# Kernel optimization log

Measured on AMD Instinct MI355X. Metric: run time of the kernel, lower is better.

Reference implementation:

```python
import jax, jax.numpy as jnp
import numpy as np

N_NODES = 50000

def setup_inputs() -> dict:
    key = jax.random.key(0)
    k1, k2, k3, k4, k5 = jax.random.split(key, 5)
    x = jax.random.normal(k1, (50000, 128), dtype=jnp.float32)
    weight = jax.random.normal(k2, (128, 32), dtype=jnp.float32) * (np.sqrt(6.0 / (128 + 32)))
    edge_src = jax.random.randint(k3, (1600000,), 0, N_NODES, dtype=jnp.int32)
    edge_dst = jax.random.randint(k4, (1600000,), 0, N_NODES, dtype=jnp.int32)
    edge_weight = jax.random.uniform(k5, (1600000,), dtype=jnp.float32)
    return {"x": x, "weight": weight, "edge_src": edge_src,
            "edge_dst": edge_dst, "edge_weight": edge_weight}

def reference(x, weight, edge_src, edge_dst, edge_weight):
    # h = x @ W  (dense GEMM)
    h = x @ weight                                   # [N, out]
    # out = spmm(adj, h): gather h rows at src, scale by edge weight,
    # scatter-add into dst rows (COO SpMM).
    msgs = edge_weight[:, None] * h[edge_src]        # [E, out]
    out = jax.ops.segment_sum(msgs, edge_dst, num_segments=N_NODES)
    return out
```

## Files before the change

### kernel.cpp

```cpp
#include <hip/hip_runtime.h>
#include <hip/hip_bf16.h>
#include <stdint.h>

#define N_NODES   50000
#define K_DIM     128
#define OUT_DIM   32
#define N_EDGES   1600000
#define NBKT      782
#define CAP       3072
#define AFIT      16
#define FB        ((N_EDGES + 256*AFIT - 1) / (256*AFIT))
#define GB        ((N_NODES + 63) / 64)
#define XSTR      136

typedef __attribute__((ext_vector_type(8))) short bf16x8;
typedef __attribute__((ext_vector_type(4))) float f32x4;

__global__ __launch_bounds__(256) void zero_cursor(int* __restrict__ cursor) {
    for (int i = threadIdx.x; i < NBKT; i += 256) cursor[i] = 0;
}

__global__ __launch_bounds__(256) void gemm_fill(const float* __restrict__ x,
                                                 const float* __restrict__ w,
                                                 __hip_bfloat16* __restrict__ h,
                                                 const int*   __restrict__ esrc,
                                                 const int*   __restrict__ edst,
                                                 const float* __restrict__ ew,
                                                 int*         __restrict__ cursor,
                                                 uint64_t*    __restrict__ pairs) {
    __shared__ __align__(16) char smem[40192];
    const int t = threadIdx.x;

    if (blockIdx.x < FB) {
        int*      cnt   = (int*)smem;
        int*      wbase = (int*)(smem + 3200);
        int*      scr   = (int*)(smem + 6400);
        uint64_t* stg   = (uint64_t*)(smem + 7424);

        for (int i = t; i < 800; i += 256) cnt[i] = 0;
        __syncthreads();

        uint32_t lo[AFIT], hi[AFIT];
        uint16_t rk[AFIT];
        const int base = blockIdx.x * 256 * AFIT;
        #pragma unroll
        for (int k = 0; k < AFIT; ++k) {
            const int e = base + k * 256 + t;
            if (e < N_EDGES) {
                const uint32_t s = (uint32_t)esrc[e];
                const uint32_t d = (uint32_t)edst[e];
                lo[k] = (d << 16) | s;
                hi[k] = __float_as_uint(ew[e]);
                rk[k] = (uint16_t)atomicAdd(&cnt[d >> 6], 1);
            } else {
                lo[k] = 0xffffffffu;
            }
        }
        __syncthreads();
        for (int i = t; i < NBKT; i += 256) {
            const int c = cnt[i];
            if (c) wbase[i] = atomicAdd(&cursor[i], c);
        }
        __syncthreads();
        int v0[4]; int lsum = 0;
        #pragma unroll
        for (int j = 0; j < 4; ++j) { v0[j] = (t * 4 + j < 800) ? cnt[t * 4 + j] : 0; lsum += v0[j]; }
        scr[t] = lsum;
        __syncthreads();
        #pragma unroll
        for (int d = 1; d < 256; d <<= 1) {
            const int a = (t >= d) ? scr[t - d] : 0;
            __syncthreads();
            scr[t] += a;
            __syncthreads();
        }
        int run = scr[t] - lsum;
        #pragma unroll
        for (int j = 0; j < 4; ++j) {
            if (t * 4 + j < 800) { const int c = v0[j]; cnt[t * 4 + j] = run; run += c; }
        }
        __syncthreads();
        #pragma unroll
        for (int k = 0; k < AFIT; ++k) {
            if (lo[k] != 0xffffffffu) {
                const int b = (int)(lo[k] >> 22);
                stg[cnt[b] + (int)rk[k]] = ((uint64_t)hi[k] << 32) | lo[k];
            }
        }
        __syncthreads();
        const int total = min(256 * AFIT, N_EDGES - base);
        for (int i = t; i < total; i += 256) {
            const uint64_t p = stg[i];
            const int b    = (int)((p >> 22) & 0x3ff);
            const int gpos = wbase[b] + i - cnt[b];
            if (gpos < CAP)
                pairs[(size_t)b * CAP + gpos] = p;
        }
    } else {
        uint16_t* wt = (uint16_t*)smem;
        uint16_t* xt = (uint16_t*)(smem + 8704);

        for (int i = t; i < K_DIM * OUT_DIM; i += 256) {
            const int k = i >> 5, c = i & 31;
            const __hip_bfloat16 bv = __float2bfloat16(w[i]);
            wt[c * XSTR + k] = *(const uint16_t*)&bv;
        }
        const int row0 = (blockIdx.x - FB) * 64;
        const float4* xg4 = reinterpret_cast<const float4*>(x);
        const long long gmax4 = (long long)N_NODES * (K_DIM / 4);
        #pragma unroll
        for (int i = 0; i < 8; ++i) {
            const int idx = i * 256 + t;
            const int row = idx >> 5;
            const int k4  = idx & 31;
            const long long gi = (long long)(row0 + row) * (K_DIM / 4) + k4;
            float4 v = make_float4(0.f, 0.f, 0.f, 0.f);
            if (gi < gmax4) v = xg4[gi];
            __hip_bfloat16 b0 = __float2bfloat16(v.x), b1 = __float2bfloat16(v.y);
            __hip_bfloat16 b2 = __float2bfloat16(v.z), b3 = __float2bfloat16(v.w);
            ushort4 u;
            u.x = *(const uint16_t*)&b0; u.y = *(const uint16_t*)&b1;
            u.z = *(const uint16_t*)&b2; u.w = *(const uint16_t*)&b3;
            *reinterpret_cast<ushort4*>(xt + row * XSTR + k4 * 4) = u;
        }
        __syncthreads();

        const int wv   = t >> 6;
        const int lane = t & 63;
        const int m    = lane & 15;
        const int kg   = lane >> 4;

        f32x4 acc0 = {0.f, 0.f, 0.f, 0.f};
        f32x4 acc1 = {0.f, 0.f, 0.f, 0.f};
        const uint16_t* arow = xt + (wv * 16 + m) * XSTR;
        const uint16_t* b0p  = wt + m * XSTR;
        const uint16_t* b1p  = wt + (16 + m) * XSTR;
        #pragma unroll
        for (int s = 0; s < 4; ++s) {
            const int k0 = s * 32 + kg * 8;
            const bf16x8 a  = *reinterpret_cast<const bf16x8*>(arow + k0);
            const bf16x8 b0 = *reinterpret_cast<const bf16x8*>(b0p + k0);
            const bf16x8 b1 = *reinterpret_cast<const bf16x8*>(b1p + k0);
            acc0 = __builtin_amdgcn_mfma_f32_16x16x32_bf16(a, b0, acc0, 0, 0, 0);
            acc1 = __builtin_amdgcn_mfma_f32_16x16x32_bf16(a, b1, acc1, 0, 0, 0);
        }
        #pragma unroll
        for (int r = 0; r < 4; ++r) {
            const int grow = row0 + wv * 16 + kg * 4 + r;
            if (grow < N_NODES) {
                h[(size_t)grow * OUT_DIM + m]      = __float2bfloat16(acc0[r]);
                h[(size_t)grow * OUT_DIM + 16 + m] = __float2bfloat16(acc1[r]);
            }
        }
    }
}

__global__ __launch_bounds__(512) void sort_pull(const int*      __restrict__ cursor,
                                                 const uint64_t* __restrict__ pairs,
                                                 const __hip_bfloat16* __restrict__ h,
                                                 float*          __restrict__ out) {
    __shared__ uint64_t stg[CAP];
    __shared__ int lcnt[64];
    __shared__ int loff[65];
    const int b    = blockIdx.x;
    const int t    = threadIdx.x;
    const size_t beg = (size_t)b * CAP;
    const int cnt  = min(cursor[b], CAP);
    const int wv   = t >> 6;
    const int lane = t & 63;
    const int cp   = lane & 15;
    const int q    = lane >> 4;

    if (t < 64) lcnt[t] = 0;
    __syncthreads();

    uint64_t pl[6];
    int      pr[6];
    #pragma unroll
    for (int k = 0; k < 6; ++k) {
        const int i = t + k * 512;
        if (i < cnt) {
            const uint64_t p = pairs[beg + i];
            const int nl = (int)((p >> 16) & 63);
            pl[k] = p;
            pr[k] = (nl << 12) | atomicAdd(&lcnt[nl], 1);
        } else {
            pr[k] = -1;
        }
    }
    __syncthreads();
    if (t < 64) {
        const int v = lcnt[t];
        int p = v;
        #pragma unroll
        for (int d = 1; d < 64; d <<= 1) {
            const int n = __shfl_up(p, d, 64);
            if (t >= d) p += n;
        }
        loff[t] = p - v;
        if (t == 63) loff[64] = p;
    }
    __syncthreads();
    #pragma unroll
    for (int k = 0; k < 6; ++k) {
        if (pr[k] >= 0)
            stg[loff[pr[k] >> 12] + (pr[k] & 0xfff)] = pl[k];
    }
    __syncthreads();

    const uint32_t* h32 = reinterpret_cast<const uint32_t*>(h);
    for (int nl = wv * 8; nl < wv * 8 + 8; ++nl) {
        const int node = (b << 6) + nl;
        if (node >= N_NODES) break;
        const int jb = loff[nl], je = loff[nl + 1];
        float ax = 0.f, ay = 0.f;
        int j = jb + q;
        for (; j + 12 < je; j += 16) {
            const uint64_t p0 = stg[j];
            const uint64_t p1 = stg[j + 4];
            const uint64_t p2 = stg[j + 8];
            const uint64_t p3 = stg[j + 12];
            const uint32_t v0 = h32[(size_t)(p0 & 0xffffu) * 16 + cp];
            const uint32_t v1 = h32[(size_t)(p1 & 0xffffu) * 16 + cp];
            const uint32_t v2 = h32[(size_t)(p2 & 0xffffu) * 16 + cp];
            const uint32_t v3 = h32[(size_t)(p3 & 0xffffu) * 16 + cp];
            const float w0 = __uint_as_float((uint32_t)(p0 >> 32));
            const float w1 = __uint_as_float((uint32_t)(p1 >> 32));
            const float w2 = __uint_as_float((uint32_t)(p2 >> 32));
            const float w3 = __uint_as_float((uint32_t)(p3 >> 32));
            ax += w0 * __uint_as_float(v0 << 16);
            ay += w0 * __uint_as_float(v0 & 0xffff0000u);
            ax += w1 * __uint_as_float(v1 << 16);
            ay += w1 * __uint_as_float(v1 & 0xffff0000u);
            ax += w2 * __uint_as_float(v2 << 16);
            ay += w2 * __uint_as_float(v2 & 0xffff0000u);
            ax += w3 * __uint_as_float(v3 << 16);
            ay += w3 * __uint_as_float(v3 & 0xffff0000u);
        }
        for (; j < je; j += 4) {
            const uint64_t p = stg[j];
            const uint32_t v = h32[(size_t)(p & 0xffffu) * 16 + cp];
            const float w = __uint_as_float((uint32_t)(p >> 32));
            ax += w * __uint_as_float(v << 16);
            ay += w * __uint_as_float(v & 0xffff0000u);
        }
        ax += __shfl_xor(ax, 16, 64);  ay += __shfl_xor(ay, 16, 64);
        ax += __shfl_xor(ax, 32, 64);  ay += __shfl_xor(ay, 32, 64);
        if (q == 0) {
            float2* o2 = reinterpret_cast<float2*>(out + (size_t)node * OUT_DIM);
            o2[cp] = make_float2(ax, ay);
        }
    }
}

__global__ __launch_bounds__(256) void gemm_only(const float* __restrict__ x,
                                                 const float* __restrict__ w,
                                                 __hip_bfloat16* __restrict__ h) {
    __shared__ float wlds[K_DIM * OUT_DIM];
    const int t = threadIdx.x;
    #pragma unroll
    for (int i = 0; i < (K_DIM * OUT_DIM) / 256; ++i)
        wlds[i * 256 + t] = w[i * 256 + t];
    __syncthreads();
    const int row = blockIdx.x * 8 + (t >> 5);
    const int col = t & 31;
    if (row >= N_NODES) return;
    const float4* x4 = reinterpret_cast<const float4*>(x + (size_t)row * K_DIM);
    float acc = 0.f;
    #pragma unroll
    for (int k4 = 0; k4 < K_DIM / 4; ++k4) {
        float4 xv = x4[k4];
        const int k = k4 * 4;
        acc += xv.x * wlds[(k + 0) * OUT_DIM + col] + xv.y * wlds[(k + 1) * OUT_DIM + col]
             + xv.z * wlds[(k + 2) * OUT_DIM + col] + xv.w * wlds[(k + 3) * OUT_DIM + col];
    }
    h[(size_t)row * OUT_DIM + col] = __float2bfloat16(acc);
}

__global__ __launch_bounds__(256) void scatter_kernel(const int*   __restrict__ esrc,
                                                      const int*   __restrict__ edst,
                                                      const float* __restrict__ ew,
                                                      const __hip_bfloat16* __restrict__ h,
                                                      float*       out) {
    const long long gid = (long long)blockIdx.x * blockDim.x + threadIdx.x;
    const int e   = (int)(gid >> 5);
    const int col = (int)(gid & 31);
    if (e >= N_EDGES) return;
    atomicAdd(out + (size_t)edst[e] * OUT_DIM + col,
              ew[e] * __bfloat162float(h[(size_t)esrc[e] * OUT_DIM + col]));
}

extern "C" void kernel_launch(void* const* d_in, const int* in_sizes, int n_in,
                              void* d_out, int out_size, void* d_ws, size_t ws_size,
                              hipStream_t stream) {
    const float* x    = (const float*)d_in[0];
    const float* w    = (const float*)d_in[1];
    const int*   esrc = (const int*)d_in[2];
    const int*   edst = (const int*)d_in[3];
    const float* ew   = (const float*)d_in[4];
    float*       out  = (float*)d_out;

    const size_t PAIRS_B = (size_t)NBKT * CAP * 8;
    const size_t H_B     = (size_t)N_NODES * OUT_DIM * 2;
    const size_t CUR_B   = (size_t)NBKT * 4;
    const size_t REQ     = PAIRS_B + H_B + CUR_B;

    uint64_t*        pairs  = (uint64_t*)d_ws;
    __hip_bfloat16*  h      = (__hip_bfloat16*)((char*)d_ws + PAIRS_B);
    int*             cursor = (int*)((char*)d_ws + PAIRS_B + H_B);

    if (ws_size >= REQ) {
        zero_cursor<<<1, 256, 0, stream>>>(cursor);
        gemm_fill<<<FB + GB, 256, 0, stream>>>(x, w, h, esrc, edst, ew, cursor, pairs);
        sort_pull<<<NBKT, 512, 0, stream>>>(cursor, pairs, h, out);
    } else {
        __hip_bfloat16* hf = (__hip_bfloat16*)d_ws;
        (void)hipMemsetAsync(d_out, 0, (size_t)out_size * sizeof(float), stream);
        gemm_only<<<(N_NODES + 7) / 8, 256, 0, stream>>>(x, w, hf);
        const long long total = (long long)N_EDGES * OUT_DIM;
        scatter_kernel<<<(int)((total + 255) / 256), 256, 0, stream>>>(esrc, edst, ew, hf, out);
    }
}
```

Measured before the change: 52.15 us.

## Fuse all stages into one persistent cooperative kernel with grid syncs

Replaces the three launches (zero cursor, gemm+fill, sort+pull) with a single cooperative kernel that loops over work items and uses grid-wide syncs between phases. Blocks grow to 512 threads, fill handles 4096 edges per item, and the GEMM splits output columns across waves. This removes per-launch overhead and inter-kernel gaps. In exchange it adds grid.sync cost, restricts the grid to the number of resident blocks (perCU*256), and drops the low-workspace fallback path.

```diff
diff --git a/kernel.cpp b/kernel.cpp
--- a/kernel.cpp
+++ b/kernel.cpp
@@ -1,6 +1,9 @@
 #include <hip/hip_runtime.h>
+#include <hip/hip_cooperative_groups.h>
 #include <hip/hip_bf16.h>
 #include <stdint.h>
+
+namespace cg = cooperative_groups;
 
 #define N_NODES   50000
 #define K_DIM     128
@@ -8,162 +11,151 @@
 #define N_EDGES   1600000
 #define NBKT      782
 #define CAP       3072
-#define AFIT      16
-#define FB        ((N_EDGES + 256*AFIT - 1) / (256*AFIT))
-#define GB        ((N_NODES + 63) / 64)
+#define FB        391
+#define GI        782
 #define XSTR      136
+#define SMEM_B    41216
 
 typedef __attribute__((ext_vector_type(8))) short bf16x8;
 typedef __attribute__((ext_vector_type(4))) float f32x4;
 
-__global__ __launch_bounds__(256) void zero_cursor(int* __restrict__ cursor) {
-    for (int i = threadIdx.x; i < NBKT; i += 256) cursor[i] = 0;
-}
-
-__global__ __launch_bounds__(256) void gemm_fill(const float* __restrict__ x,
-                                                 const float* __restrict__ w,
-                                                 __hip_bfloat16* __restrict__ h,
-                                                 const int*   __restrict__ esrc,
-                                                 const int*   __restrict__ edst,
-                                                 const float* __restrict__ ew,
-                                                 int*         __restrict__ cursor,
-                                                 uint64_t*    __restrict__ pairs) {
-    __shared__ __align__(16) char smem[40192];
-    const int t = threadIdx.x;
-
-    if (blockIdx.x < FB) {
-        int*      cnt   = (int*)smem;
-        int*      wbase = (int*)(smem + 3200);
-        int*      scr   = (int*)(smem + 6400);
-        uint64_t* stg   = (uint64_t*)(smem + 7424);
-
-        for (int i = t; i < 800; i += 256) cnt[i] = 0;
+__device__ void fill_item(int item, char* smem, int t,
+                          const int* __restrict__ esrc, const int* __restrict__ edst,
+                          const float* __restrict__ ew, int* __restrict__ cursor,
+                          uint64_t* __restrict__ pairs) {
+    int*      cnt   = (int*)smem;
+    int*      wbase = (int*)(smem + 3200);
+    int*      scr   = (int*)(smem + 6400);
+    uint64_t* stg   = (uint64_t*)(smem + 8448);
+
+    __syncthreads();
+    for (int i = t; i < 800; i += 512) cnt[i] = 0;
+    __syncthreads();
+
+    uint32_t lo[8], hi[8];
+    uint16_t rk[8];
+    const int base = item * 4096;
+    #pragma unroll
+    for (int k = 0; k < 8; ++k) {
+        const int e = base + k * 512 + t;
+        if (e < N_EDGES) {
+            const uint32_t s = (uint32_t)esrc[e];
+            const uint32_t d = (uint32_t)edst[e];
+            lo[k] = (d << 16) | s;
+            hi[k] = __float_as_uint(ew[e]);
+            rk[k] = (uint16_t)atomicAdd(&cnt[d >> 6], 1);
+        } else {
+            lo[k] = 0xffffffffu;
+        }
+    }
+    __syncthreads();
+    for (int i = t; i < NBKT; i += 512) {
+        const int c = cnt[i];
+        if (c) wbase[i] = atomicAdd(&cursor[i], c);
+    }
+    __syncthreads();
+    int v0[2]; int lsum = 0;
+    #pragma unroll
+    for (int j = 0; j < 2; ++j) { v0[j] = (t * 2 + j < 800) ? cnt[t * 2 + j] : 0; lsum += v0[j]; }
+    scr[t] = lsum;
+    __syncthreads();
+    #pragma unroll
+    for (int d = 1; d < 512; d <<= 1) {
+        const int a = (t >= d) ? scr[t - d] : 0;
         __syncthreads();
-
-        uint32_t lo[AFIT], hi[AFIT];
-        uint16_t rk[AFIT];
-        const int base = blockIdx.x * 256 * AFIT;
-        #pragma unroll
-        for (int k = 0; k < AFIT; ++k) {
-            const int e = base + k * 256 + t;
-            if (e < N_EDGES) {
-                const uint32_t s = (uint32_t)esrc[e];
-                const uint32_t d = (uint32_t)edst[e];
-                lo[k] = (d << 16) | s;
-                hi[k] = __float_as_uint(ew[e]);
-                rk[k] = (uint16_t)atomicAdd(&cnt[d >> 6], 1);
-            } else {
-                lo[k] = 0xffffffffu;
-            }
-        }
+        scr[t] += a;
         __syncthreads();
-        for (int i = t; i < NBKT; i += 256) {
-            const int c = cnt[i];
-            if (c) wbase[i] = atomicAdd(&cursor[i], c);
-        }
-        __syncthreads();
-        int v0[4]; int lsum = 0;
-        #pragma unroll
-        for (int j = 0; j < 4; ++j) { v0[j] = (t * 4 + j < 800) ? cnt[t * 4 + j] : 0; lsum += v0[j]; }
-        scr[t] = lsum;
-        __syncthreads();
-        #pragma unroll
-        for (int d = 1; d < 256; d <<= 1) {
-            const int a = (t >= d) ? scr[t - d] : 0;
-            __syncthreads();
-            scr[t] += a;
-            __syncthreads();
-        }
-        int run = scr[t] - lsum;
-        #pragma unroll
-        for (int j = 0; j < 4; ++j) {
-            if (t * 4 + j < 800) { const int c = v0[j]; cnt[t * 4 + j] = run; run += c; }
-        }
-        __syncthreads();
-        #pragma unroll
-        for (int k = 0; k < AFIT; ++k) {
-            if (lo[k] != 0xffffffffu) {
-                const int b = (int)(lo[k] >> 22);
-                stg[cnt[b] + (int)rk[k]] = ((uint64_t)hi[k] << 32) | lo[k];
-            }
-        }
-        __syncthreads();
-        const int total = min(256 * AFIT, N_EDGES - base);
-        for (int i = t; i < total; i += 256) {
-            const uint64_t p = stg[i];
-            const int b    = (int)((p >> 22) & 0x3ff);
-            const int gpos = wbase[b] + i - cnt[b];
-            if (gpos < CAP)
-                pairs[(size_t)b * CAP + gpos] = p;
-        }
-    } else {
-        uint16_t* wt = (uint16_t*)smem;
-        uint16_t* xt = (uint16_t*)(smem + 8704);
-
-        for (int i = t; i < K_DIM * OUT_DIM; i += 256) {
-            const int k = i >> 5, c = i & 31;
-            const __hip_bfloat16 bv = __float2bfloat16(w[i]);
-            wt[c * XSTR + k] = *(const uint16_t*)&bv;
-        }
-        const int row0 = (blockIdx.x - FB) * 64;
-        const float4* xg4 = reinterpret_cast<const float4*>(x);
-        const long long gmax4 = (long long)N_NODES * (K_DIM / 4);
-        #pragma unroll
-        for (int i = 0; i < 8; ++i) {
-            const int idx = i * 256 + t;
-            const int row = idx >> 5;
-            const int k4  = idx & 31;
-            const long long gi = (long long)(row0 + row) * (K_DIM / 4) + k4;
-            float4 v = make_float4(0.f, 0.f, 0.f, 0.f);
-            if (gi < gmax4) v = xg4[gi];
-            __hip_bfloat16 b0 = __float2bfloat16(v.x), b1 = __float2bfloat16(v.y);
-            __hip_bfloat16 b2 = __float2bfloat16(v.z), b3 = __float2bfloat16(v.w);
-            ushort4 u;
-            u.x = *(const uint16_t*)&b0; u.y = *(const uint16_t*)&b1;
-            u.z = *(const uint16_t*)&b2; u.w = *(const uint16_t*)&b3;
-            *reinterpret_cast<ushort4*>(xt + row * XSTR + k4 * 4) = u;
-        }
-        __syncthreads();
-
-        const int wv   = t >> 6;
-        const int lane = t & 63;
-        const int m    = lane & 15;
-        const int kg   = lane >> 4;
-
-        f32x4 acc0 = {0.f, 0.f, 0.f, 0.f};
-        f32x4 acc1 = {0.f, 0.f, 0.f, 0.f};
-        const uint16_t* arow = xt + (wv * 16 + m) * XSTR;
-        const uint16_t* b0p  = wt + m * XSTR;
-        const uint16_t* b1p  = wt + (16 + m) * XSTR;
-        #pragma unroll
-        for (int s = 0; s < 4; ++s) {
-            const int k0 = s * 32 + kg * 8;
-            const bf16x8 a  = *reinterpret_cast<const bf16x8*>(arow + k0);
-            const bf16x8 b0 = *reinterpret_cast<const bf16x8*>(b0p + k0);
-            const bf16x8 b1 = *reinterpret_cast<const bf16x8*>(b1p + k0);
-            acc0 = __builtin_amdgcn_mfma_f32_16x16x32_bf16(a, b0, acc0, 0, 0, 0);
-            acc1 = __builtin_amdgcn_mfma_f32_16x16x32_bf16(a, b1, acc1, 0, 0, 0);
-        }
-        #pragma unroll
-        for (int r = 0; r < 4; ++r) {
-            const int grow = row0 + wv * 16 + kg * 4 + r;
-            if (grow < N_NODES) {
-                h[(size_t)grow * OUT_DIM + m]      = __float2bfloat16(acc0[r]);
-                h[(size_t)grow * OUT_DIM + 16 + m] = __float2bfloat16(acc1[r]);
-            }
-        }
-    }
-}
-
-__global__ __launch_bounds__(512) void sort_pull(const int*      __restrict__ cursor,
-                                                 const uint64_t* __restrict__ pairs,
-                                                 const __hip_bfloat16* __restrict__ h,
-                                                 float*          __restrict__ out) {
-    __shared__ uint64_t stg[CAP];
-    __shared__ int lcnt[64];
-    __shared__ int loff[65];
-    const int b    = blockIdx.x;
-    const int t    = threadIdx.x;
+    }
+    int run = scr[t] - lsum;
+    #pragma unroll
+    for (int j = 0; j < 2; ++j) {
+        if (t * 2 + j < 800) { const int c = v0[j]; cnt[t * 2 + j] = run; run += c; }
+    }
+    __syncthreads();
+    #pragma unroll
+    for (int k = 0; k < 8; ++k) {
+        if (lo[k] != 0xffffffffu) {
+            const int b = (int)(lo[k] >> 22);
+            stg[cnt[b] + (int)rk[k]] = ((uint64_t)hi[k] << 32) | lo[k];
+        }
+    }
+    __syncthreads();
+    const int total = min(4096, N_EDGES - base);
+    for (int i = t; i < total; i += 512) {
+        const uint64_t p = stg[i];
+        const int b    = (int)((p >> 22) & 0x3ff);
+        const int gpos = wbase[b] + i - cnt[b];
+        if (gpos < CAP)
+            pairs[(size_t)b * CAP + gpos] = p;
+    }
+}
+
+__device__ void gemm_item(int item, char* smem, int t,
+                          const float* __restrict__ x, const float* __restrict__ w,
+                          __hip_bfloat16* __restrict__ h) {
+    uint16_t* wt = (uint16_t*)smem;
+    uint16_t* xt = (uint16_t*)(smem + 8704);
+
+    __syncthreads();
+    for (int i = t; i < K_DIM * OUT_DIM; i += 512) {
+        const int k = i >> 5, c = i & 31;
+        const __hip_bfloat16 bv = __float2bfloat16(w[i]);
+        wt[c * XSTR + k] = *(const uint16_t*)&bv;
+    }
+    const int row0 = item * 64;
+    const float4* xg4 = reinterpret_cast<const float4*>(x);
+    const long long gmax4 = (long long)N_NODES * (K_DIM / 4);
+    #pragma unroll
+    for (int i = 0; i < 4; ++i) {
+        const int idx = i * 512 + t;
+        const int row = idx >> 5;
+        const int k4  = idx & 31;
+        const long long gi = (long long)(row0 + row) * (K_DIM / 4) + k4;
+        float4 v = make_float4(0.f, 0.f, 0.f, 0.f);
+        if (gi < gmax4) v = xg4[gi];
+        __hip_bfloat16 b0 = __float2bfloat16(v.x), b1 = __float2bfloat16(v.y);
+        __hip_bfloat16 b2 = __float2bfloat16(v.z), b3 = __float2bfloat16(v.w);
+        ushort4 u;
+        u.x = *(const uint16_t*)&b0; u.y = *(const uint16_t*)&b1;
+        u.z = *(const uint16_t*)&b2; u.w = *(const uint16_t*)&b3;
+        *reinterpret_cast<ushort4*>(xt + row * XSTR + k4 * 4) = u;
+    }
+    __syncthreads();
+
+    const int wv   = t >> 6;
+    const int rt   = wv & 3;
+    const int ct   = wv >> 2;
+    const int lane = t & 63;
+    const int m    = lane & 15;
+    const int kg   = lane >> 4;
+
+    f32x4 acc = {0.f, 0.f, 0.f, 0.f};
+    const uint16_t* arow = xt + (rt * 16 + m) * XSTR;
+    const uint16_t* bp   = wt + (ct * 16 + m) * XSTR;
+    #pragma unroll
+    for (int s = 0; s < 4; ++s) {
+        const int k0 = s * 32 + kg * 8;
+        const bf16x8 a = *reinterpret_cast<const bf16x8*>(arow + k0);
+        const bf16x8 b = *reinterpret_cast<const bf16x8*>(bp + k0);
+        acc = __builtin_amdgcn_mfma_f32_16x16x32_bf16(a, b, acc, 0, 0, 0);
+    }
+    #pragma unroll
+    for (int r = 0; r < 4; ++r) {
+        const int grow = row0 + rt * 16 + kg * 4 + r;
+        if (grow < N_NODES)
+            h[(size_t)grow * OUT_DIM + ct * 16 + m] = __float2bfloat16(acc[r]);
+    }
+}
+
+__device__ void sort_item(int b, char* smem, int t,
+                          const int* __restrict__ cursor,
+                          const uint64_t* __restrict__ pairs,
+                          const __hip_bfloat16* __restrict__ h,
+                          float* __restrict__ out) {
+    uint64_t* stg  = (uint64_t*)smem;
+    int*      lcnt = (int*)(smem + 24576);
+    int*      loff = (int*)(smem + 24832);
+
     const size_t beg = (size_t)b * CAP;
     const int cnt  = min(cursor[b], CAP);
     const int wv   = t >> 6;
@@ -171,6 +163,7 @@
     const int cp   = lane & 15;
     const int q    = lane >> 4;
 
+    __syncthreads();
     if (t < 64) lcnt[t] = 0;
     __syncthreads();
 
@@ -253,41 +246,51 @@
     }
 }
 
-__global__ __launch_bounds__(256) void gemm_only(const float* __restrict__ x,
-                                                 const float* __restrict__ w,
-                                                 __hip_bfloat16* __restrict__ h) {
-    __shared__ float wlds[K_DIM * OUT_DIM];
+extern "C" __global__ __launch_bounds__(512)
+void fused_all(const float* x, const float* w, __hip_bfloat16* h,
+               const int* esrc, const int* edst, const float* ew,
+               int* cursor, uint64_t* pairs, float* out) {
+    __shared__ __align__(16) char smem[SMEM_B];
+    cg::grid_group grid = cg::this_grid();
     const int t = threadIdx.x;
-    #pragma unroll
-    for (int i = 0; i < (K_DIM * OUT_DIM) / 256; ++i)
-        wlds[i * 256 + t] = w[i * 256 + t];
-    __syncthreads();
-    const int row = blockIdx.x * 8 + (t >> 5);
-    const int col = t & 31;
-    if (row >= N_NODES) return;
-    const float4* x4 = reinterpret_cast<const float4*>(x + (size_t)row * K_DIM);
-    float acc = 0.f;
-    #pragma unroll
-    for (int k4 = 0; k4 < K_DIM / 4; ++k4) {
-        float4 xv = x4[k4];
-        const int k = k4 * 4;
-        acc += xv.x * wlds[(k + 0) * OUT_DIM + col] + xv.y * wlds[(k + 1) * OUT_DIM + col]
-             + xv.z * wlds[(k + 2) * OUT_DIM + col] + xv.w * wlds[(k + 3) * OUT_DIM + col];
-    }
-    h[(size_t)row * OUT_DIM + col] = __float2bfloat16(acc);
-}
-
-__global__ __launch_bounds__(256) void scatter_kernel(const int*   __restrict__ esrc,
-                                                      const int*   __restrict__ edst,
-                                                      const float* __restrict__ ew,
-                                                      const __hip_bfloat16* __restrict__ h,
-                                                      float*       out) {
-    const long long gid = (long long)blockIdx.x * blockDim.x + threadIdx.x;
-    const int e   = (int)(gid >> 5);
-    const int col = (int)(gid & 31);
-    if (e >= N_EDGES) return;
-    atomicAdd(out + (size_t)edst[e] * OUT_DIM + col,
-              ew[e] * __bfloat162float(h[(size_t)esrc[e] * OUT_DIM + col]));
+
+    for (int i = blockIdx.x * 512 + t; i < NBKT; i += gridDim.x * 512) cursor[i] = 0;
+    grid.sync();
+
+    for (int item = blockIdx.x; item < FB + GI; item += gridDim.x) {
+        if (item < FB) fill_item(item, smem, t, esrc, edst, ew, cursor, pairs);
+        else           gemm_item(item - FB, smem, t, x, w, h);
+    }
+    grid.sync();
+
+    for (int item = blockIdx.x; item < NBKT; item += gridDim.x)
+        sort_item(item, smem, t, cursor, pairs, h, out);
+}
+
+__global__ __launch_bounds__(256) void zero_cursor(int* __restrict__ cursor) {
+    for (int i = threadIdx.x; i < NBKT; i += 256) cursor[i] = 0;
+}
+
+__global__ __launch_bounds__(512) void gf_fill(const int* __restrict__ esrc,
+                                               const int* __restrict__ edst,
+                                               const float* __restrict__ ew,
+                                               int* __restrict__ cursor,
+                                               uint64_t* __restrict__ pairs) {
+    __shared__ __align__(16) char smem[SMEM_B];
+    fill_item(blockIdx.x, smem, threadIdx.x, esrc, edst, ew, cursor, pairs);
+}
+__global__ __launch_bounds__(512) void gf_gemm(const float* __restrict__ x,
+                                               const float* __restrict__ w,
+                                               __hip_bfloat16* __restrict__ h) {
+    __shared__ __align__(16) char smem[SMEM_B];
+    gemm_item(blockIdx.x, smem, threadIdx.x, x, w, h);
+}
+__global__ __launch_bounds__(512) void gf_sort(const int* __restrict__ cursor,
+                                               const uint64_t* __restrict__ pairs,
+                                               const __hip_bfloat16* __restrict__ h,
+                                               float* __restrict__ out) {
+    __shared__ __align__(16) char smem[SMEM_B];
+    sort_item(blockIdx.x, smem, threadIdx.x, cursor, pairs, h, out);
 }
 
 extern "C" void kernel_launch(void* const* d_in, const int* in_sizes, int n_in,
@@ -309,15 +312,25 @@
     __hip_bfloat16*  h      = (__hip_bfloat16*)((char*)d_ws + PAIRS_B);
     int*             cursor = (int*)((char*)d_ws + PAIRS_B + H_B);
 
-    if (ws_size >= REQ) {
-        zero_cursor<<<1, 256, 0, stream>>>(cursor);
-        gemm_fill<<<FB + GB, 256, 0, stream>>>(x, w, h, esrc, edst, ew, cursor, pairs);
-        sort_pull<<<NBKT, 512, 0, stream>>>(cursor, pairs, h, out);
-    } else {
-        __hip_bfloat16* hf = (__hip_bfloat16*)d_ws;
-        (void)hipMemsetAsync(d_out, 0, (size_t)out_size * sizeof(float), stream);
-        gemm_only<<<(N_NODES + 7) / 8, 256, 0, stream>>>(x, w, hf);
-        const long long total = (long long)N_EDGES * OUT_DIM;
-        scatter_kernel<<<(int)((total + 255) / 256), 256, 0, stream>>>(esrc, edst, ew, hf, out);
-    }
-}
+    if (ws_size < REQ) return;
+
+    int perCU = 0;
+    hipError_t qerr = hipOccupancyMaxActiveBlocksPerMultiprocessor(
+        &perCU, (const void*)fused_all, 512, 0);
+
+    if (qerr == hipSuccess && perCU >= 1) {
+        int grid = perCU * 256;
+        if (grid > FB + GI) grid = FB + GI;
+        void* args[] = {(void*)&x, (void*)&w, (void*)&h, (void*)&esrc,
+                        (void*)&edst, (void*)&ew, (void*)&cursor,
+                        (void*)&pairs, (void*)&out};
+        hipError_t lerr = hipLaunchCooperativeKernel(
+            (const void*)fused_all, dim3(grid), dim3(512), args, 0, stream);
+        if (lerr == hipSuccess) return;
+    }
+
+    zero_cursor<<<1, 256, 0, stream>>>(cursor);
+    gf_fill<<<FB, 512, 0, stream>>>(esrc, edst, ew, cursor, pairs);
+    gf_gemm<<<GI, 512, 0, stream>>>(x, w, h);
+    gf_sort<<<NBKT, 512, 0, stream>>>(cursor, pairs, h, out);
+}
```

After: 144.6 us. 2.77x slower.
